# Kernel tuning notes

Hardware: AMD Instinct MI355X
Metric: run time of the kernel (lower is better)

## Reference

```python
import jax, jax.numpy as jnp
import numpy as np

COND_DIM = 12 + 12 + 12 + 4 + 4          # 44
VALID_MIDI_COUNT = 128
X_DIM = 2 + VALID_MIDI_COUNT             # 130
HIDDEN = 1024
N_STEP = 16


def _uniform(key, shape, scale):
    return jax.random.uniform(key, shape, jnp.float32, -scale, scale)


def setup_inputs() -> dict:
    key = jax.random.key(0)
    ks = jax.random.split(key, 16)
    B, L = 64, 64                        # batch, length_in_bars
    z = jax.random.normal(ks[0], (B, L, HIDDEN), jnp.float32)
    x = jax.random.normal(ks[1], (B, L * N_STEP, X_DIM + COND_DIM), jnp.float32)
    s = 1.0 / np.sqrt(HIDDEN)
    in0 = X_DIM + COND_DIM               # 174, layer-0 input size
    return {
        "z": z, "x": x,
        "W_ih0": _uniform(ks[2], (4 * HIDDEN, in0), s),
        "W_hh0": _uniform(ks[3], (4 * HIDDEN, HIDDEN), s),
        "b_ih0": _uniform(ks[4], (4 * HIDDEN,), s),
        "b_hh0": _uniform(ks[5], (4 * HIDDEN,), s),
        "W_ih1": _uniform(ks[6], (4 * HIDDEN, HIDDEN), s),
        "W_hh1": _uniform(ks[7], (4 * HIDDEN, HIDDEN), s),
        "b_ih1": _uniform(ks[8], (4 * HIDDEN,), s),
        "b_hh1": _uniform(ks[9], (4 * HIDDEN,), s),
        "Wf": _uniform(ks[10], (X_DIM, HIDDEN), s),
        "bf": _uniform(ks[11], (X_DIM,), s),
    }


def _lstm_cell(inp, h, c, Wih, Whh, bih, bhh):
    # torch LSTMCell gate order: input, forget, cell(g), output
    g = inp @ Wih.T + h @ Whh.T + (bih + bhh)
    i, f, gg, o = jnp.split(g, 4, axis=1)
    c2 = jax.nn.sigmoid(f) * c + jax.nn.sigmoid(i) * jnp.tanh(gg)
    return jax.nn.sigmoid(o) * jnp.tanh(c2), c2


def reference(z, x, W_ih0, W_hh0, b_ih0, b_hh0, W_ih1, W_hh1, b_ih1, b_hh1, Wf, bf):
    B, L, H = z.shape
    Bp = B * L                                   # effective batch
    xr = x.reshape(Bp, N_STEP, x.shape[2])
    zr = z.reshape(Bp, H)
    y = jnp.swapaxes(xr[:, :, -COND_DIM:], 0, 1)  # (16, Bp, COND)

    o0 = jnp.zeros((Bp, X_DIM), z.dtype).at[:, 1].set(1.0)
    c_init = jnp.zeros((Bp, H), z.dtype)

    def step(carry, yt):
        o, h0, c0, h1, c1 = carry
        inp = jnp.concatenate([o, yt], axis=1)
        h0, c0 = _lstm_cell(inp, h0, c0, W_ih0, W_hh0, b_ih0, b_hh0)
        h1, c1 = _lstm_cell(h0, h1, c1, W_ih1, W_hh1, b_ih1, b_hh1)
        logp = jax.nn.log_softmax(h1 @ Wf.T + bf, axis=1)
        # eval-mode hard_max feedback (one-hot of argmax)
        o_next = jax.nn.one_hot(jnp.argmax(logp, axis=1), X_DIM, dtype=logp.dtype)
        return (o_next, h0, c0, h1, c1), logp

    _, logps = jax.lax.scan(step, (o0, zr, c_init, zr, c_init), y)
    # (16, Bp, X_DIM) -> (B, L*16, X_DIM)
    return jnp.swapaxes(logps, 0, 1).reshape(B, L * N_STEP, X_DIM)
```

## Files before the change

### kernel.cpp

```cpp
#include <hip/hip_runtime.h>
#include <hip/hip_bf16.h>

#define HIDDEN   1024
#define XDIM     130
#define CONDDIM  44
#define INDIM    174
#define NSTEP    16
#define BP       4096
#define K0P      1088
#define K1P      2048
#define GN       4096
#define LGN      256

typedef float f32x4 __attribute__((ext_vector_type(4)));
typedef int   i32x4 __attribute__((ext_vector_type(4)));

__device__ __forceinline__ int fused_row(int n) {
  const int q = (n >> 4) & 3;
  const int j = ((n >> 6) << 4) | (n & 15);
  return q * HIDDEN + j;
}

__device__ __forceinline__ void g2lds16(const void* g, void* l) {
  __builtin_amdgcn_global_load_lds(
      (const __attribute__((address_space(1))) void*)g,
      (__attribute__((address_space(3))) void*)l, 16, 0, 0);
}

__device__ __forceinline__ float sigm(float x)  { return 1.f / (1.f + __expf(-x)); }
__device__ __forceinline__ float tanhfast(float x) { return 2.f / (1.f + __expf(-2.f * x)) - 1.f; }

__device__ __forceinline__ signed char qscale(float v, float inv127s) {
  int q = __float2int_rn(v * inv127s);
  q = q > 127 ? 127 : (q < -127 ? -127 : q);
  return (signed char)q;
}

template<bool FB>
__global__ __launch_bounds__(512, 2)
void gemm_i8_cell_k(const signed char* __restrict__ A,
                    const signed char* __restrict__ W, int K,
                    const float* __restrict__ bcomb,
                    const float* __restrict__ SC,
                    const float* __restrict__ sA,
                    const float* __restrict__ W0T,
                    const int*   __restrict__ idx,
                    float* __restrict__ c,
                    signed char* __restrict__ d1, int ld1,
                    const float* __restrict__ sD1,
                    signed char* __restrict__ d2, int ld2)
{
  __shared__ __align__(16) signed char lds[4 * 32768];

  const int tid  = threadIdx.x;
  const int w    = tid >> 6;
  const int lane = tid & 63;
  const int bid  = blockIdx.x;
  const int swz  = ((bid & 7) << 5) | (bid >> 3);
  const int m0   = (swz >> 4) * 256;
  const int n0   = (swz & 15) * 256;
  const int wm   = w >> 2;
  const int wn   = w & 3;
  const int fr   = lane & 15;
  const int kqs  = (((lane >> 4) ^ ((fr >> 1) & 3)) * 16);
  const int sr   = lane >> 2;
  const int sc   = (((lane & 3) ^ ((sr >> 1) & 3)) * 16);
  const int NT   = K >> 6;

  i32x4 acc[8][4] = {};

  #define STAGE_A(t, d, i)                                                          \
    g2lds16(A + (size_t)(m0 + w * 32 + (i) * 16 + sr) * K + ((t) * 64 + sc),        \
            (void*)(lds + (d) * 32768 + (w * 32 + (i) * 16) * 64))
  #define STAGE_B(t, d, i)                                                          \
    g2lds16(W + (size_t)(n0 + w * 32 + (i) * 16 + sr) * K + ((t) * 64 + sc),        \
            (void*)(lds + (d) * 32768 + 16384 + (w * 32 + (i) * 16) * 64))

  const int npro = (NT < 3) ? NT : 3;
  for (int t = 0; t < npro; ++t) {
    STAGE_A(t, t, 0); STAGE_B(t, t, 0);
    STAGE_A(t, t, 1); STAGE_B(t, t, 1);
  }
  if (NT >= 3)      asm volatile("s_waitcnt vmcnt(8)" ::: "memory");
  else if (NT == 2) asm volatile("s_waitcnt vmcnt(4)" ::: "memory");
  else              asm volatile("s_waitcnt vmcnt(0)" ::: "memory");
  __builtin_amdgcn_s_barrier();

  for (int t = 0; t < NT; ++t) {
    const int d  = t & 3;
    const signed char* As = lds + d * 32768;
    const signed char* Bs = As + 16384;
    const int tp = t + 3;
    const int dp = tp & 3;
    const bool pf = tp < NT;

    i32x4 bfr[4];
    #pragma unroll
    for (int nf = 0; nf < 4; ++nf)
      bfr[nf] = *reinterpret_cast<const i32x4*>(&Bs[(wn * 64 + nf * 16 + fr) * 64 + kqs]);

    #pragma unroll
    for (int half = 0; half < 2; ++half) {
      if (pf) {
        if (half == 0) { STAGE_A(tp, dp, 0); STAGE_A(tp, dp, 1); }
        else           { STAGE_B(tp, dp, 0); STAGE_B(tp, dp, 1); }
      }
      i32x4 afr[4];
      #pragma unroll
      for (int q = 0; q < 4; ++q)
        afr[q] = *reinterpret_cast<const i32x4*>(&As[(wm * 128 + (half * 4 + q) * 16 + fr) * 64 + kqs]);
      __builtin_amdgcn_s_setprio(1);
      #pragma unroll
      for (int q = 0; q < 4; ++q)
        #pragma unroll
        for (int nf = 0; nf < 4; ++nf)
          acc[half * 4 + q][nf] =
              __builtin_amdgcn_mfma_i32_16x16x64_i8(afr[q], bfr[nf], acc[half * 4 + q][nf], 0, 0, 0);
      __builtin_amdgcn_s_setprio(0);
    }

    if (t + 3 < NT)      asm volatile("s_waitcnt vmcnt(8)" ::: "memory");
    else if (t + 2 < NT) asm volatile("s_waitcnt vmcnt(4)" ::: "memory");
    else if (t + 1 < NT) asm volatile("s_waitcnt vmcnt(0)" ::: "memory");
    if (t + 1 < NT) __builtin_amdgcn_s_barrier();
  }
  #undef STAGE_A
  #undef STAGE_B

  const int fq = lane >> 4;
  const int cb = n0 + wn * 64;
  const int j  = ((cb >> 6) << 4) | fr;

  const float bs0 = bcomb[cb + fr],      sc0 = SC[cb + fr];
  const float bs1 = bcomb[cb + 16 + fr], sc1 = SC[cb + 16 + fr];
  const float bs2 = bcomb[cb + 32 + fr], sc2 = SC[cb + 32 + fr];
  const float bs3 = bcomb[cb + 48 + fr], sc3 = SC[cb + 48 + fr];

  #pragma unroll
  for (int mf = 0; mf < 8; ++mf) {
    #pragma unroll
    for (int r = 0; r < 4; ++r) {
      const int b = m0 + wm * 128 + mf * 16 + fq * 4 + r;
      const float sa = sA ? sA[b] : 1.f;
      float gi = (float)acc[mf][0][r] * (sc0 * sa) + bs0;
      float gf = (float)acc[mf][1][r] * (sc1 * sa) + bs1;
      float gg = (float)acc[mf][2][r] * (sc2 * sa) + bs2;
      float go = (float)acc[mf][3][r] * (sc3 * sa) + bs3;
      if (FB) {
        const float* wr = W0T + (size_t)idx[b] * GN;
        gi += wr[cb + fr];
        gf += wr[cb + 16 + fr];
        gg += wr[cb + 32 + fr];
        go += wr[cb + 48 + fr];
      }
      const size_t ci = (size_t)b * HIDDEN + j;
      const float cn = sigm(gf) * c[ci] + sigm(gi) * tanhfast(gg);
      c[ci] = cn;
      const float hn = sigm(go) * tanhfast(cn);
      if (d1) {
        const float i127s = sD1 ? (127.f / sD1[b]) : 127.f;
        d1[(size_t)b * ld1 + j] = qscale(hn, i127s);
      }
      if (d2) d2[(size_t)b * ld2 + j] = qscale(hn, 127.f);
    }
  }
}

__global__ __launch_bounds__(256, 4)
void logits_i8_k(const signed char* __restrict__ A, int lda,
                 const signed char* __restrict__ Wfi,
                 const float* __restrict__ SCf,
                 float* __restrict__ C, int ldc)
{
  __shared__ __align__(16) signed char As[64 * 64];
  __shared__ __align__(16) signed char Bs[128 * 64];

  const int tid  = threadIdx.x;
  const int w    = tid >> 6;
  const int lane = tid & 63;
  const int m0 = blockIdx.y * 64;
  const int n0 = blockIdx.x * 128;
  const int wm = w >> 1;
  const int wn = w & 1;
  const int fr = lane & 15;
  const int kqs = (((lane >> 4) ^ ((fr >> 1) & 3)) * 16);
  const int sr  = lane >> 2;
  const int sc  = (((lane & 3) ^ ((sr >> 1) & 3)) * 16);

  i32x4 acc[2][4] = {};

  for (int k0 = 0; k0 < HIDDEN; k0 += 64) {
    __syncthreads();
    g2lds16(A + (size_t)(m0 + w * 16 + sr) * lda + (k0 + sc), (void*)(As + (w * 16) * 64));
    g2lds16(Wfi + (size_t)(n0 + w * 16 + sr) * HIDDEN + (k0 + sc), (void*)(Bs + (w * 16) * 64));
    g2lds16(Wfi + (size_t)(n0 + 64 + w * 16 + sr) * HIDDEN + (k0 + sc), (void*)(Bs + (64 + w * 16) * 64));
    __syncthreads();

    i32x4 af[2], bw[4];
    #pragma unroll
    for (int i = 0; i < 2; ++i)
      af[i] = *reinterpret_cast<const i32x4*>(&As[(wm * 32 + i * 16 + fr) * 64 + kqs]);
    #pragma unroll
    for (int j = 0; j < 4; ++j)
      bw[j] = *reinterpret_cast<const i32x4*>(&Bs[(wn * 64 + j * 16 + fr) * 64 + kqs]);
    #pragma unroll
    for (int i = 0; i < 2; ++i)
      #pragma unroll
      for (int j = 0; j < 4; ++j)
        acc[i][j] = __builtin_amdgcn_mfma_i32_16x16x64_i8(af[i], bw[j], acc[i][j], 0, 0, 0);
  }

  const int fq = lane >> 4;
  #pragma unroll
  for (int i = 0; i < 2; ++i)
    #pragma unroll
    for (int j = 0; j < 4; ++j) {
      const int col = n0 + wn * 64 + j * 16 + fr;
      const float scf = SCf[col];
      #pragma unroll
      for (int r = 0; r < 4; ++r) {
        const int row = m0 + wm * 32 + i * 16 + fq * 4 + r;
        C[(size_t)row * ldc + col] = (float)acc[i][j][r] * scf;
      }
    }
}

__global__ void smax_k(const float* __restrict__ LG,
                       const float* __restrict__ bfv,
                       float* __restrict__ out, int t,
                       const float* __restrict__ x,
                       signed char* __restrict__ A0next,
                       int* __restrict__ idx)
{
  const int b    = blockIdx.x;
  const int lane = threadIdx.x;
  const float NINF = -__builtin_inff();
  const float* lg = LG + (size_t)b * LGN;

  const int c1 = lane + 64, c2 = lane + 128;
  float v0 = lg[lane] + bfv[lane];
  float v1 = lg[c1] + bfv[c1];
  float v2 = (c2 < XDIM) ? lg[c2] + bfv[c2] : NINF;

  float m = fmaxf(v0, fmaxf(v1, v2));
  #pragma unroll
  for (int o = 32; o > 0; o >>= 1) m = fmaxf(m, __shfl_xor(m, o, 64));

  int bi = 0x7fffffff;
  if (v0 == m) bi = lane;
  if (v1 == m) bi = min(bi, c1);
  if (v2 == m) bi = min(bi, c2);
  #pragma unroll
  for (int o = 32; o > 0; o >>= 1) bi = min(bi, __shfl_xor(bi, o, 64));

  float s = __expf(v0 - m) + __expf(v1 - m) + ((c2 < XDIM) ? __expf(v2 - m) : 0.f);
  #pragma unroll
  for (int o = 32; o > 0; o >>= 1) s += __shfl_xor(s, o, 64);
  const float lse = __logf(s);

  float* orow = out + ((size_t)b * NSTEP + t) * XDIM;
  orow[lane] = v0 - m - lse;
  orow[c1]   = v1 - m - lse;
  if (c2 < XDIM) orow[c2] = v2 - m - lse;
  if (lane == 0) idx[b] = bi;

  if (t + 1 < NSTEP) {
    const float yv = (lane < CONDDIM)
        ? x[((size_t)b * NSTEP + (t + 1)) * INDIM + XDIM + lane] : 0.f;
    A0next[(size_t)b * K0P + HIDDEN + lane] = qscale(yv * 0.25f, 127.f);
  }
}

__global__ void initq_k(const float* __restrict__ z, const float* __restrict__ x,
                        float* __restrict__ c0, float* __restrict__ c1,
                        signed char* __restrict__ A0, signed char* __restrict__ A1,
                        float* __restrict__ S0, float* __restrict__ S1,
                        int* __restrict__ idx)
{
  const int b    = blockIdx.x;
  const int lane = threadIdx.x;
  const float* zr = z + (size_t)b * HIDDEN;

  float mz = 0.f;
  for (int k = lane; k < HIDDEN; k += 64) mz = fmaxf(mz, fabsf(zr[k]));
  #pragma unroll
  for (int o = 32; o > 0; o >>= 1) mz = fmaxf(mz, __shfl_xor(mz, o, 64));

  const float yv = (lane < CONDDIM) ? x[((size_t)b * NSTEP) * INDIM + XDIM + lane] : 0.f;
  float my = fabsf(yv) * 0.25f;
  #pragma unroll
  for (int o = 32; o > 0; o >>= 1) my = fmaxf(my, __shfl_xor(my, o, 64));

  const float s0 = fmaxf(fmaxf(mz, my), 1e-6f);
  const float s1 = fmaxf(mz, 1.f);
  const float i0 = 127.f / s0;
  const float i1 = 127.f / s1;

  for (int k = lane; k < HIDDEN; k += 64) {
    const float zv = zr[k];
    A0[(size_t)b * K0P + k]          = qscale(zv, i0);
    A1[(size_t)b * K1P + HIDDEN + k] = qscale(zv, i1);
    c0[(size_t)b * HIDDEN + k] = 0.f;
    c1[(size_t)b * HIDDEN + k] = 0.f;
  }
  A0[(size_t)b * K0P + HIDDEN + lane] = qscale(yv * 0.25f, i0);
  if (lane == 0) { S0[b] = s0; S1[b] = s1; idx[b] = 1; }
}

__global__ void rowmax0_k(const float* __restrict__ Wih0, const float* __restrict__ Whh0,
                          float* __restrict__ RM, float* __restrict__ SC)
{
  const int n = blockIdx.x, lane = threadIdx.x;
  const int row = fused_row(n);
  float m = 1e-20f;
  for (int k = lane; k < HIDDEN; k += 64)  m = fmaxf(m, fabsf(Whh0[(size_t)row * HIDDEN + k]));
  for (int k = lane; k < CONDDIM; k += 64) m = fmaxf(m, 4.f * fabsf(Wih0[(size_t)row * INDIM + XDIM + k]));
  #pragma unroll
  for (int o = 32; o > 0; o >>= 1) m = fmaxf(m, __shfl_xor(m, o, 64));
  if (lane == 0) { RM[n] = m; SC[n] = m / 16129.f; }
}

__global__ void rowmax1_k(const float* __restrict__ Wih1, const float* __restrict__ Whh1,
                          float* __restrict__ RM, float* __restrict__ SC)
{
  const int n = blockIdx.x, lane = threadIdx.x;
  const int row = fused_row(n);
  float m = 1e-20f;
  for (int k = lane; k < HIDDEN; k += 64) {
    m = fmaxf(m, fabsf(Wih1[(size_t)row * HIDDEN + k]));
    m = fmaxf(m, fabsf(Whh1[(size_t)row * HIDDEN + k]));
  }
  #pragma unroll
  for (int o = 32; o > 0; o >>= 1) m = fmaxf(m, __shfl_xor(m, o, 64));
  if (lane == 0) { RM[n] = m; SC[n] = m / 16129.f; }
}

__global__ void packi0_k(const float* __restrict__ Wih0, const float* __restrict__ Whh0,
                         const float* __restrict__ RM, signed char* __restrict__ Bp)
{
  const int t = blockIdx.x * blockDim.x + threadIdx.x;
  if (t >= GN * K0P) return;
  const int n = t / K0P, k = t % K0P;
  const int row = fused_row(n);
  float v = 0.f;
  if (k < HIDDEN)                v = Whh0[(size_t)row * HIDDEN + k];
  else if (k < HIDDEN + CONDDIM) v = 4.f * Wih0[(size_t)row * INDIM + XDIM + (k - HIDDEN)];
  Bp[t] = qscale(v, 127.f / RM[n]);
}

__global__ void packi1_k(const float* __restrict__ Wih1, const float* __restrict__ Whh1,
                         const float* __restrict__ RM, signed char* __restrict__ Bp)
{
  const int t = blockIdx.x * blockDim.x + threadIdx.x;
  if (t >= GN * K1P) return;
  const int n = t >> 11, k = t & 2047;
  const int row = fused_row(n);
  const float v = (k < HIDDEN) ? Wih1[(size_t)row * HIDDEN + k]
                               : Whh1[(size_t)row * HIDDEN + (k - HIDDEN)];
  Bp[t] = qscale(v, 127.f / RM[n]);
}

__global__ void packbias_k(const float* __restrict__ bih, const float* __restrict__ bhh,
                           float* __restrict__ bc)
{
  const int n = blockIdx.x * blockDim.x + threadIdx.x;
  if (n >= GN) return;
  const int row = fused_row(n);
  bc[n] = bih[row] + bhh[row];
}

__global__ void rowmaxf_k(const float* __restrict__ Wf, float* __restrict__ RM,
                          float* __restrict__ SC)
{
  const int n = blockIdx.x, lane = threadIdx.x;
  float m = 1e-20f;
  if (n < XDIM)
    for (int k = lane; k < HIDDEN; k += 64) m = fmaxf(m, fabsf(Wf[(size_t)n * HIDDEN + k]));
  else m = 1.f;
  #pragma unroll
  for (int o = 32; o > 0; o >>= 1) m = fmaxf(m, __shfl_xor(m, o, 64));
  if (lane == 0) { RM[n] = m; SC[n] = m / 16129.f; }
}

__global__ void packfi_k(const float* __restrict__ Wf, const float* __restrict__ RM,
                         signed char* __restrict__ Wfi)
{
  const int t = blockIdx.x * blockDim.x + threadIdx.x;
  if (t >= LGN * HIDDEN) return;
  const int r = t >> 10, k = t & 1023;
  const float v = (r < XDIM) ? Wf[(size_t)r * HIDDEN + k] : 0.f;
  Wfi[t] = qscale(v, 127.f / RM[r]);
}

__global__ void packt_k(const float* __restrict__ Wih0, float* __restrict__ W0T)
{
  const int t = blockIdx.x * blockDim.x + threadIdx.x;
  if (t >= XDIM * GN) return;
  const int e = t >> 12, n = t & 4095;
  W0T[t] = Wih0[(size_t)fused_row(n) * INDIM + e];
}

extern "C" void kernel_launch(void* const* d_in, const int* in_sizes, int n_in,
                              void* d_out, int out_size, void* d_ws, size_t ws_size,
                              hipStream_t stream)
{
  const float* z    = (const float*)d_in[0];
  const float* x    = (const float*)d_in[1];
  const float* Wih0 = (const float*)d_in[2];
  const float* Whh0 = (const float*)d_in[3];
  const float* bih0 = (const float*)d_in[4];
  const float* bhh0 = (const float*)d_in[5];
  const float* Wih1 = (const float*)d_in[6];
  const float* Whh1 = (const float*)d_in[7];
  const float* bih1 = (const float*)d_in[8];
  const float* bhh1 = (const float*)d_in[9];
  const float* Wf   = (const float*)d_in[10];
  const float* bfv  = (const float*)d_in[11];
  float* out = (float*)d_out;

  char* ws = (char*)d_ws;
  size_t off = 0;
  auto alloc = [&](size_t bytes) { void* p = ws + off; off += (bytes + 255) & ~(size_t)255; return p; };

  float*       LG    = (float*)      alloc((size_t)BP * LGN * 4);
  signed char* A0i8a = (signed char*)alloc((size_t)BP * K0P);
  signed char* A0i8b = (signed char*)alloc((size_t)BP * K0P);
  signed char* A1i8a = (signed char*)alloc((size_t)BP * K1P);
  signed char* A1i8b = (signed char*)alloc((size_t)BP * K1P);
  signed char* Bpi0  = (signed char*)alloc((size_t)GN * K0P);
  signed char* Bpi1  = (signed char*)alloc((size_t)GN * K1P);
  signed char* Wfi   = (signed char*)alloc((size_t)LGN * HIDDEN);
  float*       W0T   = (float*)      alloc((size_t)XDIM * GN * 4);
  float*       bc0   = (float*)      alloc((size_t)GN * 4);
  float*       bc1   = (float*)      alloc((size_t)GN * 4);
  float*       RM0   = (float*)      alloc((size_t)GN * 4);
  float*       SC0   = (float*)      alloc((size_t)GN * 4);
  float*       RM1   = (float*)      alloc((size_t)GN * 4);
  float*       SC1   = (float*)      alloc((size_t)GN * 4);
  float*       RMf   = (float*)      alloc((size_t)LGN * 4);
  float*       SCf   = (float*)      alloc((size_t)LGN * 4);
  float*       S0    = (float*)      alloc((size_t)BP * 4);
  float*       S1    = (float*)      alloc((size_t)BP * 4);
  float*       c0    = (float*)      alloc((size_t)BP * HIDDEN * 4);
  float*       c1    = (float*)      alloc((size_t)BP * HIDDEN * 4);
  int*         idx   = (int*)        alloc((size_t)BP * 4);
  (void)ws_size; (void)in_sizes; (void)n_in; (void)out_size;

  rowmax0_k<<<GN, 64, 0, stream>>>(Wih0, Whh0, RM0, SC0);
  rowmax1_k<<<GN, 64, 0, stream>>>(Wih1, Whh1, RM1, SC1);
  rowmaxf_k<<<LGN, 64, 0, stream>>>(Wf, RMf, SCf);
  packi0_k<<<(GN * K0P + 255) / 256, 256, 0, stream>>>(Wih0, Whh0, RM0, Bpi0);
  packi1_k<<<(GN * K1P + 255) / 256, 256, 0, stream>>>(Wih1, Whh1, RM1, Bpi1);
  packfi_k<<<(LGN * HIDDEN + 255) / 256, 256, 0, stream>>>(Wf, RMf, Wfi);
  packbias_k<<<(GN + 255) / 256, 256, 0, stream>>>(bih0, bhh0, bc0);
  packbias_k<<<(GN + 255) / 256, 256, 0, stream>>>(bih1, bhh1, bc1);
  packt_k<<<(XDIM * GN + 255) / 256, 256, 0, stream>>>(Wih0, W0T);
  initq_k<<<BP, 64, 0, stream>>>(z, x, c0, c1, A0i8a, A1i8a, S0, S1, idx);

  for (int t = 0; t < NSTEP; ++t) {
    signed char* A0c = (t & 1) ? A0i8b : A0i8a;
    signed char* A0n = (t & 1) ? A0i8a : A0i8b;
    signed char* A1c = (t & 1) ? A1i8b : A1i8a;
    signed char* A1n = (t & 1) ? A1i8a : A1i8b;
    const float* sA0 = (t == 0) ? S0 : nullptr;
    const float* sA1 = (t == 0) ? S1 : nullptr;
    const float* sD1 = (t == 0) ? S1 : nullptr;

    gemm_i8_cell_k<true><<<256, 512, 0, stream>>>(
        A0c, Bpi0, K0P, bc0, SC0, sA0, W0T, idx, c0,
        A1c, K1P, sD1,
        A0n, K0P);
    gemm_i8_cell_k<false><<<256, 512, 0, stream>>>(
        A1c, Bpi1, K1P, bc1, SC1, sA1, nullptr, nullptr, c1,
        A1n + HIDDEN, K1P, nullptr,
        nullptr, 0);
    logits_i8_k<<<dim3(LGN / 128, BP / 64), dim3(256), 0, stream>>>(
        A1n + HIDDEN, K1P, Wfi, SCf, LG, LGN);
    smax_k<<<BP, 64, 0, stream>>>(LG, bfv, out, t, x, A0n, idx);
  }
}
```

Baseline: 1.705 ms.

## Store LSTM cell state in fp16 and prefetch it during final K tiles

The cell-state buffers drop from fp32 to fp16, which halves the read/write traffic of the cell update in each gate GEMM epilogue. The old cell values are also loaded into registers four K-tiles before the main loop ends, so their latency overlaps the remaining MFMA work. The vmcnt wait counts are raised to account for the extra outstanding loads. The risks are accuracy loss from fp16 cell state accumulating over 16 steps, and higher register pressure from 32 extra floats per thread under launch bounds of 512x2.

```diff
diff --git a/kernel.cpp b/kernel.cpp
--- a/kernel.cpp
+++ b/kernel.cpp
@@ -45,7 +45,7 @@
                     const float* __restrict__ sA,
                     const float* __restrict__ W0T,
                     const int*   __restrict__ idx,
-                    float* __restrict__ c,
+                    _Float16* __restrict__ c,
                     signed char* __restrict__ d1, int ld1,
                     const float* __restrict__ sD1,
                     signed char* __restrict__ d2, int ld2)
@@ -67,7 +67,12 @@
   const int sc   = (((lane & 3) ^ ((sr >> 1) & 3)) * 16);
   const int NT   = K >> 6;
 
+  const int fq = lane >> 4;
+  const int cb = n0 + wn * 64;
+  const int j  = ((cb >> 6) << 4) | fr;
+
   i32x4 acc[8][4] = {};
+  float cpre[8][4] = {};
 
   #define STAGE_A(t, d, i)                                                          \
     g2lds16(A + (size_t)(m0 + w * 32 + (i) * 16 + sr) * K + ((t) * 64 + sc),        \
@@ -119,17 +124,29 @@
       __builtin_amdgcn_s_setprio(0);
     }
 
-    if (t + 3 < NT)      asm volatile("s_waitcnt vmcnt(8)" ::: "memory");
-    else if (t + 2 < NT) asm volatile("s_waitcnt vmcnt(4)" ::: "memory");
-    else if (t + 1 < NT) asm volatile("s_waitcnt vmcnt(0)" ::: "memory");
-    if (t + 1 < NT) __builtin_amdgcn_s_barrier();
+    if (t + 4 == NT) {
+      #pragma unroll
+      for (int mf = 0; mf < 8; ++mf)
+        #pragma unroll
+        for (int r = 0; r < 4; ++r) {
+          const int b = m0 + wm * 128 + mf * 16 + fq * 4 + r;
+          cpre[mf][r] = (float)c[(size_t)b * HIDDEN + j];
+        }
+      asm volatile("s_waitcnt vmcnt(40)" ::: "memory");
+      __builtin_amdgcn_s_barrier();
+    } else if (t + 3 < NT) {
+      asm volatile("s_waitcnt vmcnt(8)" ::: "memory");
+      __builtin_amdgcn_s_barrier();
+    } else if (t + 3 == NT) {
+      asm volatile("s_waitcnt vmcnt(36)" ::: "memory");
+      __builtin_amdgcn_s_barrier();
+    } else if (t + 2 == NT) {
+      asm volatile("s_waitcnt vmcnt(32)" ::: "memory");
+      __builtin_amdgcn_s_barrier();
+    }
   }
   #undef STAGE_A
   #undef STAGE_B
-
-  const int fq = lane >> 4;
-  const int cb = n0 + wn * 64;
-  const int j  = ((cb >> 6) << 4) | fr;
 
   const float bs0 = bcomb[cb + fr],      sc0 = SC[cb + fr];
   const float bs1 = bcomb[cb + 16 + fr], sc1 = SC[cb + 16 + fr];
@@ -154,8 +171,10 @@
         go += wr[cb + 48 + fr];
       }
       const size_t ci = (size_t)b * HIDDEN + j;
-      const float cn = sigm(gf) * c[ci] + sigm(gi) * tanhfast(gg);
-      c[ci] = cn;
+      float cold = cpre[mf][r];
+      if (NT < 4) cold = (float)c[ci];
+      const float cn = sigm(gf) * cold + sigm(gi) * tanhfast(gg);
+      c[ci] = (_Float16)cn;
       const float hn = sigm(go) * tanhfast(cn);
       if (d1) {
         const float i127s = sD1 ? (127.f / sD1[b]) : 127.f;
@@ -272,7 +291,7 @@
 }
 
 __global__ void initq_k(const float* __restrict__ z, const float* __restrict__ x,
-                        float* __restrict__ c0, float* __restrict__ c1,
+                        _Float16* __restrict__ c0, _Float16* __restrict__ c1,
                         signed char* __restrict__ A0, signed char* __restrict__ A1,
                         float* __restrict__ S0, float* __restrict__ S1,
                         int* __restrict__ idx)
@@ -300,8 +319,8 @@
     const float zv = zr[k];
     A0[(size_t)b * K0P + k]          = qscale(zv, i0);
     A1[(size_t)b * K1P + HIDDEN + k] = qscale(zv, i1);
-    c0[(size_t)b * HIDDEN + k] = 0.f;
-    c1[(size_t)b * HIDDEN + k] = 0.f;
+    c0[(size_t)b * HIDDEN + k] = (_Float16)0.f;
+    c1[(size_t)b * HIDDEN + k] = (_Float16)0.f;
   }
   A0[(size_t)b * K0P + HIDDEN + lane] = qscale(yv * 0.25f, i0);
   if (lane == 0) { S0[b] = s0; S1[b] = s1; idx[b] = 1; }
@@ -441,8 +460,8 @@
   float*       SCf   = (float*)      alloc((size_t)LGN * 4);
   float*       S0    = (float*)      alloc((size_t)BP * 4);
   float*       S1    = (float*)      alloc((size_t)BP * 4);
-  float*       c0    = (float*)      alloc((size_t)BP * HIDDEN * 4);
-  float*       c1    = (float*)      alloc((size_t)BP * HIDDEN * 4);
+  _Float16*    c0    = (_Float16*)   alloc((size_t)BP * HIDDEN * 2);
+  _Float16*    c1    = (_Float16*)   alloc((size_t)BP * HIDDEN * 2);
   int*         idx   = (int*)        alloc((size_t)BP * 4);
   (void)ws_size; (void)in_sizes; (void)n_in; (void)out_size;
 
```

Result: slower. 1.950 ms (+14.4%).

## Shrink LSTM GEMM tiles to 128x128 and split activation buffers per source

Applied to the files above, without the earlier changes.

The fused int8 GEMM+cell kernel moves from 256x256 tiles with 512 threads and a 4-stage LDS pipeline to 128x128 tiles with 256 threads, a 2-stage double buffer and 1024 blocks, which should give better occupancy and wave balance across the CUs. Concatenated activation buffers are replaced by separate hidden-state and condition arrays. The K loop now takes its A tiles from two source pointers, and the cell state is stored in a blocked transposed layout. The trade-off is a shallower prefetch pipeline and more redundant reads of A and B tiles because each tile is smaller.

```diff
diff --git a/kernel.cpp b/kernel.cpp
--- a/kernel.cpp
+++ b/kernel.cpp
@@ -11,6 +11,7 @@
 #define K1P      2048
 #define GN       4096
 #define LGN      256
+#define SPLITK   16
 
 typedef float f32x4 __attribute__((ext_vector_type(4)));
 typedef int   i32x4 __attribute__((ext_vector_type(4)));
@@ -37,110 +38,106 @@
 }
 
 template<bool FB>
-__global__ __launch_bounds__(512, 2)
-void gemm_i8_cell_k(const signed char* __restrict__ A,
+__global__ __launch_bounds__(256, 3)
+void gemm_i8_cell_k(const signed char* __restrict__ Alo,
+                    const signed char* __restrict__ Ahi, int ahstr,
                     const signed char* __restrict__ W, int K,
                     const float* __restrict__ bcomb,
                     const float* __restrict__ SC,
                     const float* __restrict__ sA,
                     const float* __restrict__ W0T,
                     const int*   __restrict__ idx,
-                    float* __restrict__ c,
-                    signed char* __restrict__ d1, int ld1,
-                    const float* __restrict__ sD1,
-                    signed char* __restrict__ d2, int ld2)
-{
-  __shared__ __align__(16) signed char lds[4 * 32768];
+                    float* __restrict__ cT,
+                    signed char* __restrict__ d1,
+                    signed char* __restrict__ d2,
+                    const float* __restrict__ sD2)
+{
+  __shared__ __align__(16) signed char lds[2 * 16384];
 
   const int tid  = threadIdx.x;
   const int w    = tid >> 6;
   const int lane = tid & 63;
   const int bid  = blockIdx.x;
-  const int swz  = ((bid & 7) << 5) | (bid >> 3);
-  const int m0   = (swz >> 4) * 256;
-  const int n0   = (swz & 15) * 256;
-  const int wm   = w >> 2;
-  const int wn   = w & 3;
+  const int swz  = ((bid & 7) << 7) | (bid >> 3);
+  const int m0   = (swz >> 5) * 128;
+  const int n0   = (swz & 31) * 128;
+  const int wm   = w >> 1;
+  const int wn   = w & 1;
   const int fr   = lane & 15;
   const int kqs  = (((lane >> 4) ^ ((fr >> 1) & 3)) * 16);
   const int sr   = lane >> 2;
   const int sc   = (((lane & 3) ^ ((sr >> 1) & 3)) * 16);
   const int NT   = K >> 6;
 
-  i32x4 acc[8][4] = {};
-
-  #define STAGE_A(t, d, i)                                                          \
-    g2lds16(A + (size_t)(m0 + w * 32 + (i) * 16 + sr) * K + ((t) * 64 + sc),        \
-            (void*)(lds + (d) * 32768 + (w * 32 + (i) * 16) * 64))
-  #define STAGE_B(t, d, i)                                                          \
-    g2lds16(W + (size_t)(n0 + w * 32 + (i) * 16 + sr) * K + ((t) * 64 + sc),        \
-            (void*)(lds + (d) * 32768 + 16384 + (w * 32 + (i) * 16) * 64))
-
-  const int npro = (NT < 3) ? NT : 3;
-  for (int t = 0; t < npro; ++t) {
-    STAGE_A(t, t, 0); STAGE_B(t, t, 0);
-    STAGE_A(t, t, 1); STAGE_B(t, t, 1);
-  }
-  if (NT >= 3)      asm volatile("s_waitcnt vmcnt(8)" ::: "memory");
-  else if (NT == 2) asm volatile("s_waitcnt vmcnt(4)" ::: "memory");
-  else              asm volatile("s_waitcnt vmcnt(0)" ::: "memory");
-  __builtin_amdgcn_s_barrier();
-
-  for (int t = 0; t < NT; ++t) {
-    const int d  = t & 3;
-    const signed char* As = lds + d * 32768;
-    const signed char* Bs = As + 16384;
-    const int tp = t + 3;
-    const int dp = tp & 3;
-    const bool pf = tp < NT;
-
-    i32x4 bfr[4];
-    #pragma unroll
-    for (int nf = 0; nf < 4; ++nf)
-      bfr[nf] = *reinterpret_cast<const i32x4*>(&Bs[(wn * 64 + nf * 16 + fr) * 64 + kqs]);
-
-    #pragma unroll
-    for (int half = 0; half < 2; ++half) {
-      if (pf) {
-        if (half == 0) { STAGE_A(tp, dp, 0); STAGE_A(tp, dp, 1); }
-        else           { STAGE_B(tp, dp, 0); STAGE_B(tp, dp, 1); }
-      }
-      i32x4 afr[4];
-      #pragma unroll
-      for (int q = 0; q < 4; ++q)
-        afr[q] = *reinterpret_cast<const i32x4*>(&As[(wm * 128 + (half * 4 + q) * 16 + fr) * 64 + kqs]);
-      __builtin_amdgcn_s_setprio(1);
-      #pragma unroll
-      for (int q = 0; q < 4; ++q)
-        #pragma unroll
-        for (int nf = 0; nf < 4; ++nf)
-          acc[half * 4 + q][nf] =
-              __builtin_amdgcn_mfma_i32_16x16x64_i8(afr[q], bfr[nf], acc[half * 4 + q][nf], 0, 0, 0);
-      __builtin_amdgcn_s_setprio(0);
-    }
-
-    if (t + 3 < NT)      asm volatile("s_waitcnt vmcnt(8)" ::: "memory");
-    else if (t + 2 < NT) asm volatile("s_waitcnt vmcnt(4)" ::: "memory");
-    else if (t + 1 < NT) asm volatile("s_waitcnt vmcnt(0)" ::: "memory");
-    if (t + 1 < NT) __builtin_amdgcn_s_barrier();
-  }
-  #undef STAGE_A
-  #undef STAGE_B
-
   const int fq = lane >> 4;
   const int cb = n0 + wn * 64;
   const int j  = ((cb >> 6) << 4) | fr;
+
+  i32x4 acc[4][4] = {};
+
+  auto stA = [&](int t, int buf) {
+    const signed char* ab; size_t astr; int koff;
+    if (t < SPLITK) { ab = Alo; astr = 1024;          koff = t * 64; }
+    else            { ab = Ahi; astr = (size_t)ahstr; koff = (t - SPLITK) * 64; }
+    #pragma unroll
+    for (int i = 0; i < 2; ++i)
+      g2lds16(ab + (size_t)(m0 + w * 32 + i * 16 + sr) * astr + (koff + sc),
+              (void*)(lds + buf * 16384 + (w * 32 + i * 16) * 64));
+  };
+  auto stB = [&](int t, int buf) {
+    #pragma unroll
+    for (int i = 0; i < 2; ++i)
+      g2lds16(W + (size_t)(n0 + w * 32 + i * 16 + sr) * K + (t * 64 + sc),
+              (void*)(lds + buf * 16384 + 8192 + (w * 32 + i * 16) * 64));
+  };
+
+  stA(0, 0); stB(0, 0);
+  stA(1, 1); stB(1, 1);
+  asm volatile("s_waitcnt vmcnt(4)" ::: "memory");
+  __builtin_amdgcn_s_barrier();
+
+  for (int t = 0; t < NT; ++t) {
+    const int buf = t & 1;
+    const signed char* As = lds + buf * 16384;
+    const signed char* Bs = As + 8192;
+
+    i32x4 afr[4], bfr[4];
+    #pragma unroll
+    for (int q = 0; q < 4; ++q)
+      afr[q] = *reinterpret_cast<const i32x4*>(&As[(wm * 64 + q * 16 + fr) * 64 + kqs]);
+    #pragma unroll
+    for (int nf = 0; nf < 4; ++nf)
+      bfr[nf] = *reinterpret_cast<const i32x4*>(&Bs[(wn * 64 + nf * 16 + fr) * 64 + kqs]);
+    asm volatile("s_waitcnt lgkmcnt(0)" ::: "memory");
+    __builtin_amdgcn_s_barrier();
+    if (t + 2 < NT) { stA(t + 2, buf); stB(t + 2, buf); }
+
+    __builtin_amdgcn_s_setprio(1);
+    #pragma unroll
+    for (int q = 0; q < 4; ++q)
+      #pragma unroll
+      for (int nf = 0; nf < 4; ++nf)
+        acc[q][nf] = __builtin_amdgcn_mfma_i32_16x16x64_i8(afr[q], bfr[nf], acc[q][nf], 0, 0, 0);
+    __builtin_amdgcn_s_setprio(0);
+
+    if (t + 1 < NT) {
+      if (t + 2 < NT) asm volatile("s_waitcnt vmcnt(4)" ::: "memory");
+      else            asm volatile("s_waitcnt vmcnt(0)" ::: "memory");
+      __builtin_amdgcn_s_barrier();
+    }
+  }
 
   const float bs0 = bcomb[cb + fr],      sc0 = SC[cb + fr];
   const float bs1 = bcomb[cb + 16 + fr], sc1 = SC[cb + 16 + fr];
   const float bs2 = bcomb[cb + 32 + fr], sc2 = SC[cb + 32 + fr];
   const float bs3 = bcomb[cb + 48 + fr], sc3 = SC[cb + 48 + fr];
-
-  #pragma unroll
-  for (int mf = 0; mf < 8; ++mf) {
+  const size_t ctbase = (size_t)(j >> 5) * ((size_t)BP * 32) + (j & 31);
+
+  #pragma unroll
+  for (int mf = 0; mf < 4; ++mf) {
     #pragma unroll
     for (int r = 0; r < 4; ++r) {
-      const int b = m0 + wm * 128 + mf * 16 + fq * 4 + r;
+      const int b = m0 + wm * 64 + mf * 16 + fq * 4 + r;
       const float sa = sA ? sA[b] : 1.f;
       float gi = (float)acc[mf][0][r] * (sc0 * sa) + bs0;
       float gf = (float)acc[mf][1][r] * (sc1 * sa) + bs1;
@@ -153,15 +150,12 @@
         gg += wr[cb + 32 + fr];
         go += wr[cb + 48 + fr];
       }
-      const size_t ci = (size_t)b * HIDDEN + j;
-      const float cn = sigm(gf) * c[ci] + sigm(gi) * tanhfast(gg);
-      c[ci] = cn;
+      const size_t ci = ctbase + (size_t)b * 32;
+      const float cn = sigm(gf) * cT[ci] + sigm(gi) * tanhfast(gg);
+      cT[ci] = cn;
       const float hn = sigm(go) * tanhfast(cn);
-      if (d1) {
-        const float i127s = sD1 ? (127.f / sD1[b]) : 127.f;
-        d1[(size_t)b * ld1 + j] = qscale(hn, i127s);
-      }
-      if (d2) d2[(size_t)b * ld2 + j] = qscale(hn, 127.f);
+      d1[(size_t)b * 1024 + j] = qscale(hn, 127.f);
+      if (d2) d2[(size_t)b * 1024 + j] = qscale(hn, 127.f / sD2[b]);
     }
   }
 }
@@ -201,26 +195,26 @@
     for (int i = 0; i < 2; ++i)
       af[i] = *reinterpret_cast<const i32x4*>(&As[(wm * 32 + i * 16 + fr) * 64 + kqs]);
     #pragma unroll
-    for (int j = 0; j < 4; ++j)
-      bw[j] = *reinterpret_cast<const i32x4*>(&Bs[(wn * 64 + j * 16 + fr) * 64 + kqs]);
+    for (int jn = 0; jn < 4; ++jn)
+      bw[jn] = *reinterpret_cast<const i32x4*>(&Bs[(wn * 64 + jn * 16 + fr) * 64 + kqs]);
     #pragma unroll
     for (int i = 0; i < 2; ++i)
       #pragma unroll
-      for (int j = 0; j < 4; ++j)
-        acc[i][j] = __builtin_amdgcn_mfma_i32_16x16x64_i8(af[i], bw[j], acc[i][j], 0, 0, 0);
+      for (int jn = 0; jn < 4; ++jn)
+        acc[i][jn] = __builtin_amdgcn_mfma_i32_16x16x64_i8(af[i], bw[jn], acc[i][jn], 0, 0, 0);
   }
 
   const int fq = lane >> 4;
   #pragma unroll
   for (int i = 0; i < 2; ++i)
     #pragma unroll
-    for (int j = 0; j < 4; ++j) {
-      const int col = n0 + wn * 64 + j * 16 + fr;
+    for (int jn = 0; jn < 4; ++jn) {
+      const int col = n0 + wn * 64 + jn * 16 + fr;
       const float scf = SCf[col];
       #pragma unroll
       for (int r = 0; r < 4; ++r) {
         const int row = m0 + wm * 32 + i * 16 + fq * 4 + r;
-        C[(size_t)row * ldc + col] = (float)acc[i][j][r] * scf;
+        C[(size_t)row * ldc + col] = (float)acc[i][jn][r] * scf;
       }
     }
 }
@@ -229,7 +223,7 @@
                        const float* __restrict__ bfv,
                        float* __restrict__ out, int t,
                        const float* __restrict__ x,
-                       signed char* __restrict__ A0next,
+                       signed char* __restrict__ Y,
                        int* __restrict__ idx)
 {
   const int b    = blockIdx.x;
@@ -267,13 +261,15 @@
   if (t + 1 < NSTEP) {
     const float yv = (lane < CONDDIM)
         ? x[((size_t)b * NSTEP + (t + 1)) * INDIM + XDIM + lane] : 0.f;
-    A0next[(size_t)b * K0P + HIDDEN + lane] = qscale(yv * 0.25f, 127.f);
+    Y[(size_t)b * 64 + lane] = qscale(yv * 0.25f, 127.f);
   }
 }
 
 __global__ void initq_k(const float* __restrict__ z, const float* __restrict__ x,
-                        float* __restrict__ c0, float* __restrict__ c1,
-                        signed char* __restrict__ A0, signed char* __restrict__ A1,
+                        float* __restrict__ c0T, float* __restrict__ c1T,
+                        signed char* __restrict__ Hz0,
+                        signed char* __restrict__ Hz1,
+                        signed char* __restrict__ Y,
                         float* __restrict__ S0, float* __restrict__ S1,
                         int* __restrict__ idx)
 {
@@ -298,12 +294,13 @@
 
   for (int k = lane; k < HIDDEN; k += 64) {
     const float zv = zr[k];
-    A0[(size_t)b * K0P + k]          = qscale(zv, i0);
-    A1[(size_t)b * K1P + HIDDEN + k] = qscale(zv, i1);
-    c0[(size_t)b * HIDDEN + k] = 0.f;
-    c1[(size_t)b * HIDDEN + k] = 0.f;
-  }
-  A0[(size_t)b * K0P + HIDDEN + lane] = qscale(yv * 0.25f, i0);
+    Hz0[(size_t)b * 1024 + k] = qscale(zv, i0);
+    Hz1[(size_t)b * 1024 + k] = qscale(zv, i1);
+    const size_t ci = (size_t)(k >> 5) * ((size_t)BP * 32) + (size_t)b * 32 + (k & 31);
+    c0T[ci] = 0.f;
+    c1T[ci] = 0.f;
+  }
+  Y[(size_t)b * 64 + lane] = qscale(yv * 0.25f, i0);
   if (lane == 0) { S0[b] = s0; S1[b] = s1; idx[b] = 1; }
 }
 
@@ -422,28 +419,30 @@
   size_t off = 0;
   auto alloc = [&](size_t bytes) { void* p = ws + off; off += (bytes + 255) & ~(size_t)255; return p; };
 
-  float*       LG    = (float*)      alloc((size_t)BP * LGN * 4);
-  signed char* A0i8a = (signed char*)alloc((size_t)BP * K0P);
-  signed char* A0i8b = (signed char*)alloc((size_t)BP * K0P);
-  signed char* A1i8a = (signed char*)alloc((size_t)BP * K1P);
-  signed char* A1i8b = (signed char*)alloc((size_t)BP * K1P);
-  signed char* Bpi0  = (signed char*)alloc((size_t)GN * K0P);
-  signed char* Bpi1  = (signed char*)alloc((size_t)GN * K1P);
-  signed char* Wfi   = (signed char*)alloc((size_t)LGN * HIDDEN);
-  float*       W0T   = (float*)      alloc((size_t)XDIM * GN * 4);
-  float*       bc0   = (float*)      alloc((size_t)GN * 4);
-  float*       bc1   = (float*)      alloc((size_t)GN * 4);
-  float*       RM0   = (float*)      alloc((size_t)GN * 4);
-  float*       SC0   = (float*)      alloc((size_t)GN * 4);
-  float*       RM1   = (float*)      alloc((size_t)GN * 4);
-  float*       SC1   = (float*)      alloc((size_t)GN * 4);
-  float*       RMf   = (float*)      alloc((size_t)LGN * 4);
-  float*       SCf   = (float*)      alloc((size_t)LGN * 4);
-  float*       S0    = (float*)      alloc((size_t)BP * 4);
-  float*       S1    = (float*)      alloc((size_t)BP * 4);
-  float*       c0    = (float*)      alloc((size_t)BP * HIDDEN * 4);
-  float*       c1    = (float*)      alloc((size_t)BP * HIDDEN * 4);
-  int*         idx   = (int*)        alloc((size_t)BP * 4);
+  float*       LG   = (float*)      alloc((size_t)BP * LGN * 4);
+  signed char* H0a  = (signed char*)alloc((size_t)BP * 1024);
+  signed char* H0b  = (signed char*)alloc((size_t)BP * 1024);
+  signed char* H0s1 = (signed char*)alloc((size_t)BP * 1024);
+  signed char* H1a  = (signed char*)alloc((size_t)BP * 1024);
+  signed char* H1b  = (signed char*)alloc((size_t)BP * 1024);
+  signed char* Y    = (signed char*)alloc((size_t)BP * 64);
+  signed char* Bpi0 = (signed char*)alloc((size_t)GN * K0P);
+  signed char* Bpi1 = (signed char*)alloc((size_t)GN * K1P);
+  signed char* Wfi  = (signed char*)alloc((size_t)LGN * HIDDEN);
+  float*       W0T  = (float*)      alloc((size_t)XDIM * GN * 4);
+  float*       bc0  = (float*)      alloc((size_t)GN * 4);
+  float*       bc1  = (float*)      alloc((size_t)GN * 4);
+  float*       RM0  = (float*)      alloc((size_t)GN * 4);
+  float*       SC0  = (float*)      alloc((size_t)GN * 4);
+  float*       RM1  = (float*)      alloc((size_t)GN * 4);
+  float*       SC1  = (float*)      alloc((size_t)GN * 4);
+  float*       RMf  = (float*)      alloc((size_t)LGN * 4);
+  float*       SCf  = (float*)      alloc((size_t)LGN * 4);
+  float*       S0   = (float*)      alloc((size_t)BP * 4);
+  float*       S1   = (float*)      alloc((size_t)BP * 4);
+  float*       c0T  = (float*)      alloc((size_t)BP * HIDDEN * 4);
+  float*       c1T  = (float*)      alloc((size_t)BP * HIDDEN * 4);
+  int*         idx  = (int*)        alloc((size_t)BP * 4);
   (void)ws_size; (void)in_sizes; (void)n_in; (void)out_size;
 
   rowmax0_k<<<GN, 64, 0, stream>>>(Wih0, Whh0, RM0, SC0);
@@ -455,27 +454,25 @@
   packbias_k<<<(GN + 255) / 256, 256, 0, stream>>>(bih0, bhh0, bc0);
   packbias_k<<<(GN + 255) / 256, 256, 0, stream>>>(bih1, bhh1, bc1);
   packt_k<<<(XDIM * GN + 255) / 256, 256, 0, stream>>>(Wih0, W0T);
-  initq_k<<<BP, 64, 0, stream>>>(z, x, c0, c1, A0i8a, A1i8a, S0, S1, idx);
+  initq_k<<<BP, 64, 0, stream>>>(z, x, c0T, c1T, H0b, H1b, Y, S0, S1, idx);
 
   for (int t = 0; t < NSTEP; ++t) {
-    signed char* A0c = (t & 1) ? A0i8b : A0i8a;
-    signed char* A0n = (t & 1) ? A0i8a : A0i8b;
-    signed char* A1c = (t & 1) ? A1i8b : A1i8a;
-    signed char* A1n = (t & 1) ? A1i8a : A1i8b;
-    const float* sA0 = (t == 0) ? S0 : nullptr;
-    const float* sA1 = (t == 0) ? S1 : nullptr;
-    const float* sD1 = (t == 0) ? S1 : nullptr;
-
-    gemm_i8_cell_k<true><<<256, 512, 0, stream>>>(
-        A0c, Bpi0, K0P, bc0, SC0, sA0, W0T, idx, c0,
-        A1c, K1P, sD1,
-        A0n, K0P);
-    gemm_i8_cell_k<false><<<256, 512, 0, stream>>>(
-        A1c, Bpi1, K1P, bc1, SC1, sA1, nullptr, nullptr, c1,
-        A1n + HIDDEN, K1P, nullptr,
-        nullptr, 0);
+    signed char* H0cur  = (t & 1) ? H0b : H0a;
+    signed char* H0prev = (t & 1) ? H0a : H0b;
+    signed char* H1cur  = (t & 1) ? H1b : H1a;
+    signed char* H1prev = (t & 1) ? H1a : H1b;
+
+    gemm_i8_cell_k<true><<<1024, 256, 0, stream>>>(
+        H0prev, Y, 64, Bpi0, K0P, bc0, SC0,
+        (t == 0) ? S0 : nullptr, W0T, idx, c0T,
+        H0cur,
+        (t == 0) ? H0s1 : nullptr, S1);
+    gemm_i8_cell_k<false><<<1024, 256, 0, stream>>>(
+        (t == 0) ? H0s1 : H0cur, H1prev, 1024, Bpi1, K1P, bc1, SC1,
+        (t == 0) ? S1 : nullptr, nullptr, nullptr, c1T,
+        H1cur, nullptr, nullptr);
     logits_i8_k<<<dim3(LGN / 128, BP / 64), dim3(256), 0, stream>>>(
-        A1n + HIDDEN, K1P, Wfi, SCf, LG, LGN);
-    smax_k<<<BP, 64, 0, stream>>>(LG, bfv, out, t, x, A0n, idx);
-  }
-}
+        H1cur, 1024, Wfi, SCf, LG, LGN);
+    smax_k<<<BP, 64, 0, stream>>>(LG, bfv, out, t, x, Y, idx);
+  }
+}
```

Measured after the change: 1.700 ms. Within noise of the previous version (-0.3%).
